# Optimization experiments

Measured on AMD Instinct MI355X. Metric: run time of the kernel, lower is better.

## Reference

```python
import jax, jax.numpy as jnp
import numpy as np

NEG = -1e30  # finite stand-in for -inf so logsumexp grads stay finite


def ctc_loss_mean(y_true, log_probs_tm, input_length, label_length, blank=0):
    """CTC loss (forward algorithm in log space), mean over batch.

    log_probs_tm: [T, B, C] time-major log-probabilities.
    y_true:       [B, L] dense int labels (blank=0 excluded from real labels).
    """
    T, B, C = log_probs_tm.shape
    L = y_true.shape[1]
    S = 2 * L + 1  # extended label length: blank, l1, blank, l2, ...
    ll = jnp.clip(label_length, 1, L)
    il = jnp.clip(input_length, 1, T)

    # Extended label sequence: blanks at even positions, labels at odd.
    ext = jnp.full((B, S), blank, dtype=jnp.int32).at[:, 1::2].set(y_true.astype(jnp.int32))
    ext_m2 = jnp.concatenate([jnp.full((B, 2), -1, jnp.int32), ext[:, :-2]], axis=1)
    # Skip transition (s-2 -> s) allowed only for label positions with no repeat.
    allow_skip = ((jnp.arange(S) % 2 == 1)[None, :]) & (ext != ext_m2)

    lp0 = jnp.take_along_axis(log_probs_tm[0], ext, axis=1)  # [B, S]
    alpha0 = jnp.full((B, S), NEG, log_probs_tm.dtype)
    alpha0 = alpha0.at[:, 0].set(lp0[:, 0]).at[:, 1].set(lp0[:, 1])

    def step(alpha, xs):
        lp_t, t = xs
        lpe = jnp.take_along_axis(lp_t, ext, axis=1)  # [B, S]
        a1 = jnp.concatenate([jnp.full((B, 1), NEG, alpha.dtype), alpha[:, :-1]], axis=1)
        a2 = jnp.concatenate([jnp.full((B, 2), NEG, alpha.dtype), alpha[:, :-2]], axis=1)
        a2 = jnp.where(allow_skip, a2, NEG)
        new = jax.nn.logsumexp(jnp.stack([alpha, a1, a2]), axis=0) + lpe
        # Freeze alpha once past each example's input_length.
        return jnp.where((t < il)[:, None], new, alpha), None

    alpha, _ = jax.lax.scan(step, alpha0, (log_probs_tm[1:], jnp.arange(1, T)))

    # Loss = -log(alpha[2*ll-1] + alpha[2*ll]) at the final (frozen) time step.
    idx = jnp.stack([2 * ll - 1, 2 * ll], axis=1)  # [B, 2]
    end_vals = jnp.take_along_axis(alpha, idx, axis=1)
    loss = -jax.nn.logsumexp(end_vals, axis=1)
    return jnp.mean(loss)


def setup_inputs() -> dict:
    key = jax.random.key(0)
    kx, kl, ki, kj = jax.random.split(key, 4)
    B, T, C, L = 64, 1024, 128, 256
    # y_pred are probabilities (module applies log), so softmax random logits.
    y_pred = jax.nn.softmax(jax.random.normal(kx, (B, T, C), jnp.float32), axis=-1)
    y_true = jax.random.randint(kl, (B, L), 1, C, jnp.int32)  # blank=0 excluded
    input_length = jax.random.randint(ki, (B,), T // 2, T + 1, jnp.int32)
    label_length = jax.random.randint(kj, (B,), L // 2, L + 1, jnp.int32)
    return {"y_true": y_true, "y_pred": y_pred,
            "input_length": input_length, "label_length": label_length}


def reference(y_true, y_pred, input_length, label_length):
    # Mirror CTCLayer.call: log + transpose to time-major, reshape lengths.
    log_tm = jnp.log(jnp.transpose(y_pred, (1, 0, 2)))  # [T, B, C]
    loss = ctc_loss_mean(y_true, log_tm,
                         input_length.reshape(-1), label_length.reshape(-1),
                         blank=0)
    return log_tm, loss
```

## Files before the change

kernel.cpp:

```cpp
#include <hip/hip_runtime.h>
#include <math.h>

constexpr int B = 64;
constexpr int T = 1024;
constexpr int C = 128;
constexpr int L = 256;
constexpr int S = 2 * L + 1;
constexpr int TRB = 2048;

template <int N> struct IC { static constexpr int value = N; };

__device__ __forceinline__ float shr1(float x) {
#if __has_builtin(__builtin_amdgcn_mov_dpp)
    return __int_as_float(__builtin_amdgcn_mov_dpp(
        __float_as_int(x), 0x138 , 0xf, 0xf, true));
#else
    return __int_as_float(__builtin_amdgcn_update_dpp(
        0, __float_as_int(x), 0x138, 0xf, 0xf, true));
#endif
}

template <int CTRL>
__device__ __forceinline__ float maxdpp(float x) {
#if __has_builtin(__builtin_amdgcn_mov_dpp)
    float t = __int_as_float(__builtin_amdgcn_mov_dpp(
        __float_as_int(x), CTRL, 0xf, 0xf, true));
#else
    float t = __int_as_float(__builtin_amdgcn_update_dpp(
        0, __float_as_int(x), CTRL, 0xf, 0xf, true));
#endif
    return fmaxf(x, t);
}

__device__ __forceinline__ float wave_max_dpp(float x) {
    x = maxdpp<0x111>(x);
    x = maxdpp<0x112>(x);
    x = maxdpp<0x114>(x);
    x = maxdpp<0x118>(x);
    x = maxdpp<0x142>(x);
    x = maxdpp<0x143>(x);
    return __int_as_float(__builtin_amdgcn_readlane(__float_as_int(x), 63));
}

__global__
__attribute__((amdgpu_waves_per_eu(1, 1)))
__launch_bounds__(64)
void ctc_fused(
    const float* __restrict__ yp,
    const int*   __restrict__ yt,
    const int*   __restrict__ il_,
    const int*   __restrict__ ll_,
    float* __restrict__ out_log,
    float* __restrict__ out_loss)
{
    const int lane = threadIdx.x;
    if (blockIdx.x >= B) {
        int id = blockIdx.x - B;
        int bb = id >> 5;
        int ck = id & 31;
        const float4* src = (const float4*)yp + ((size_t)bb * T + ck * 32) * 32;
        float4* o4 = (float4*)out_log;
        #pragma unroll
        for (int k = 0; k < 16; ++k) {
            int o = k * 64 + lane;
            float4 v = src[o];
            int tt = ck * 32 + (o >> 5);
            int c4 = o & 31;
            float4 r;
            r.x = __logf(v.x); r.y = __logf(v.y);
            r.z = __logf(v.z); r.w = __logf(v.w);
            o4[((size_t)tt * B + bb) * 32 + c4] = r;
        }
        return;
    }

    const int b = blockIdx.x;

    __shared__ float afin[S];

    int il = il_[b]; il = min(max(il, 1), T);
    int ll = ll_[b]; ll = min(max(ll, 1), L);
    const float* yb = yp + (size_t)b * T * C;

    int4 y4  = *(const int4*)(yt + b * L + 4 * lane);
    int  po  = lane ? 4 * lane - 4 : 0;
    int4 py4 = *(const int4*)(yt + b * L + po);
    int  ppw = yt[b * L + (lane >= 2 ? 4 * lane - 5 : 0)];

    int lab[8]   = {py4.x, py4.y, py4.z, py4.w, y4.x, y4.y, y4.z, y4.w};
    int labm1[8] = {ppw,   py4.x, py4.y, py4.z, py4.w, y4.x, y4.y, y4.z};
    float skf[8];
    #pragma unroll
    for (int k = 0; k < 8; ++k)
        skf[k] = ((4 * lane + k >= 5) && (lab[k] != labm1[k])) ? 1.f : 0.f;

    const int c0 = y4.x, c1 = y4.y, c2 = y4.z, c3 = y4.w;

    int z0;
    asm volatile("v_mov_b32 %0, 0" : "=v"(z0));

    float gv[3][4][4], gbv[3][4];

    auto fill = [&](auto Qc, int r0) {
        constexpr int Q = decltype(Qc)::value;
        #pragma unroll
        for (int j = 0; j < 4; ++j) {
            int r = r0 + j; r = r < T ? r : T - 1;
            const float* rb = yb + (size_t)r * C;
            gbv[Q][j]   = rb[z0];
            gv[Q][j][0] = rb[c0];
            gv[Q][j][1] = rb[c1];
            gv[Q][j][2] = rb[c2];
            gv[Q][j][3] = rb[c3];
        }
    };

    float p00 = yb[0];
    float p0l = yb[c0];

    fill(IC<0>{}, 1);
    fill(IC<1>{}, 5);

    float w[17];
    #pragma unroll
    for (int i = 0; i < 17; ++i) w[i] = 0.f;
    if (lane == 0) { w[8] = p00; w[9] = p0l; }

    auto halo = [&]() {
        #pragma unroll
        for (int k = 0; k < 8; ++k) w[k] = shr1(w[8 + k]);
    };
    halo();

    int lsi = 0;
    int t0 = 0;

    auto group = [&](auto Pc) {
        constexpr int P = decltype(Pc)::value;
        constexpr int F = (P + 2) % 3;
        float g1[4], g2[4], g3[4];
        #pragma unroll
        for (int j = 0; j < 4; ++j) {
            g1[j] = shr1(gv[P][j][1]);
            g2[j] = shr1(gv[P][j][2]);
            g3[j] = shr1(gv[P][j][3]);
        }
        #pragma unroll
        for (int j = 0; j < 4; ++j) {
            #pragma unroll
            for (int i = 16; i >= 2 * (j + 1); --i) {
                float acc = w[i] + w[i - 1];
                float g;
                if (i & 1) {
                    const int k = (i - 1) >> 1;
                    acc = fmaf(skf[k], w[i - 2], acc);
                    g = (k >= 4) ? gv[P][j][k - 4]
                                 : (k == 1 ? g1[j] : (k == 2 ? g2[j] : g3[j]));
                } else {
                    g = gbv[P][j];
                }
                w[i] = acc * g;
            }
        }
        fill(IC<F>{}, t0 + 9);
        __builtin_amdgcn_sched_barrier(0x7);
        halo();
        t0 += 4;
    };

    auto maxw = [&]() {
        return fmaxf(fmaxf(fmaxf(w[8], w[9]), fmaxf(w[10], w[11])),
                     fmaxf(fmaxf(w[12], w[13]),
                           fmaxf(fmaxf(w[14], w[15]), w[16])));
    };

    int pinv_bits = 127 << 23;
    int psh = 0;
    auto measure = [&]() {
        float mm = wave_max_dpp(maxw());
        int eb = (__float_as_int(mm) >> 23) & 0xff;
        int sh = 350 - eb;
        sh = sh > 254 ? 254 : (sh < 1 ? 1 : sh);
        pinv_bits = sh << 23;
        psh = sh - 127;
    };
    auto apply = [&]() {
        float inv = __int_as_float(pinv_bits);
        #pragma unroll
        for (int i = 0; i < 17; ++i) w[i] *= inv;
        lsi -= psh;
    };
    auto rescale = [&]() { measure(); apply(); };

    const int full_end = ((il - 1) >> 2) << 2;

    while (t0 + 24 <= full_end) {
        group(IC<0>{});
        apply();
        group(IC<1>{});
        measure();
        group(IC<2>{});
        apply();
        group(IC<0>{});
        measure();
        group(IC<1>{});
        apply();
        group(IC<2>{});
        measure();
    }
    apply();

    if (t0 + 4 <= full_end) { group(IC<0>{}); rescale(); }
    if (t0 + 4 <= full_end) { group(IC<1>{}); rescale(); }
    if (t0 + 4 <= full_end) { group(IC<2>{}); rescale(); }
    if (t0 + 4 <= full_end) { group(IC<0>{}); rescale(); }
    if (t0 + 4 <= full_end) { group(IC<1>{}); }

    const int ph = (full_end >> 2) % 3;
    float tg[3][4], tb[3];
    switch (ph) {
    case 0:
        #pragma unroll
        for (int j = 0; j < 3; ++j) { tb[j]=gbv[0][j]; tg[j][0]=gv[0][j][0]; tg[j][1]=gv[0][j][1]; tg[j][2]=gv[0][j][2]; tg[j][3]=gv[0][j][3]; }
        break;
    case 1:
        #pragma unroll
        for (int j = 0; j < 3; ++j) { tb[j]=gbv[1][j]; tg[j][0]=gv[1][j][0]; tg[j][1]=gv[1][j][1]; tg[j][2]=gv[1][j][2]; tg[j][3]=gv[1][j][3]; }
        break;
    default:
        #pragma unroll
        for (int j = 0; j < 3; ++j) { tb[j]=gbv[2][j]; tg[j][0]=gv[2][j][0]; tg[j][1]=gv[2][j][1]; tg[j][2]=gv[2][j][2]; tg[j][3]=gv[2][j][3]; }
        break;
    }
    #pragma unroll
    for (int j = 0; j < 3; ++j) {
        int r = full_end + 1 + j;
        if (r < il) {
            float hh = shr1(w[15]);
            float gb = tb[j];
            float n8  = (w[8] + hh) * gb;
            float n9  = fmaf(skf[4], hh,    w[9]  + w[8])  * tg[j][0];
            float n10 = (w[10] + w[9])  * gb;
            float n11 = fmaf(skf[5], w[9],  w[11] + w[10]) * tg[j][1];
            float n12 = (w[12] + w[11]) * gb;
            float n13 = fmaf(skf[6], w[11], w[13] + w[12]) * tg[j][2];
            float n14 = (w[14] + w[13]) * gb;
            float n15 = fmaf(skf[7], w[13], w[15] + w[14]) * tg[j][3];
            float n16 = (w[16] + w[15]) * gb;
            w[8] = n8;  w[9] = n9;  w[10] = n10; w[11] = n11; w[12] = n12;
            w[13] = n13; w[14] = n14; w[15] = n15; w[16] = n16;
        }
    }

    #pragma unroll
    for (int k = 0; k < 8; ++k) afin[8 * lane + k] = w[8 + k];
    if (lane == 63) afin[512] = w[16];
    __syncthreads();
    if (lane == 0) {
        float e1 = afin[2 * ll - 1];
        float e2 = afin[2 * ll];
        float sum = fmaxf(e1 + e2, 1e-37f);
        float loss = -(__log2f(sum) + (float)lsi) * 0.6931471805599453f;
        atomicAdd(out_loss, loss * (1.0f / (float)B));
    }
}

extern "C" void kernel_launch(void* const* d_in, const int* in_sizes, int n_in,
                              void* d_out, int out_size, void* d_ws, size_t ws_size,
                              hipStream_t stream) {
    const int*   y_true = (const int*)d_in[0];
    const float* y_pred = (const float*)d_in[1];
    const int*   in_len = (const int*)d_in[2];
    const int*   lb_len = (const int*)d_in[3];

    float* out_log  = (float*)d_out;
    float* out_loss = (float*)d_out + (size_t)T * B * C;

    hipMemsetAsync(out_loss, 0, sizeof(float), stream);
    ctc_fused<<<B + TRB, 64, 0, stream>>>(y_pred, y_true, in_len, lb_len,
                                          out_log, out_loss);
}
```

Before: 177.4 us.

## Replace 4-step halo window recursion with per-step DPP neighbor shuffle

Each group used to recompute a 17-wide overlapping window, doing redundant halo work across 4 time steps, then refreshed 8 halo values and 3×4 gathered probabilities with DPP shifts. The main loop now runs a 9-value per-step update that fetches one neighbor value per step with a DPP shift. This cuts the redundant arithmetic by roughly half. The cost is one cross-lane dependency per step on the serial critical path, where before there was one per four steps. Row loads now use a single clamped base pointer with constant offsets, and the tail selection shifts its indices to match.

```diff
diff --git a/kernel.cpp b/kernel.cpp
--- a/kernel.cpp
+++ b/kernel.cpp
@@ -82,17 +82,13 @@
     int ll = ll_[b]; ll = min(max(ll, 1), L);
     const float* yb = yp + (size_t)b * T * C;
 
-    int4 y4  = *(const int4*)(yt + b * L + 4 * lane);
-    int  po  = lane ? 4 * lane - 4 : 0;
-    int4 py4 = *(const int4*)(yt + b * L + po);
-    int  ppw = yt[b * L + (lane >= 2 ? 4 * lane - 5 : 0)];
-
-    int lab[8]   = {py4.x, py4.y, py4.z, py4.w, y4.x, y4.y, y4.z, y4.w};
-    int labm1[8] = {ppw,   py4.x, py4.y, py4.z, py4.w, y4.x, y4.y, y4.z};
-    float skf[8];
-    #pragma unroll
-    for (int k = 0; k < 8; ++k)
-        skf[k] = ((4 * lane + k >= 5) && (lab[k] != labm1[k])) ? 1.f : 0.f;
+    int4 y4 = *(const int4*)(yt + b * L + 4 * lane);
+    int  pw = yt[b * L + (lane ? 4 * lane - 1 : 0)];
+
+    float skf4 = (lane && (y4.x != pw))   ? 1.f : 0.f;
+    float skf5 = (y4.y != y4.x) ? 1.f : 0.f;
+    float skf6 = (y4.z != y4.y) ? 1.f : 0.f;
+    float skf7 = (y4.w != y4.z) ? 1.f : 0.f;
 
     const int c0 = y4.x, c1 = y4.y, c2 = y4.z, c3 = y4.w;
 
@@ -103,15 +99,15 @@
 
     auto fill = [&](auto Qc, int r0) {
         constexpr int Q = decltype(Qc)::value;
+        int r = r0 < T - 4 ? r0 : T - 4;
+        const float* rb = yb + (size_t)r * C;
         #pragma unroll
         for (int j = 0; j < 4; ++j) {
-            int r = r0 + j; r = r < T ? r : T - 1;
-            const float* rb = yb + (size_t)r * C;
-            gbv[Q][j]   = rb[z0];
-            gv[Q][j][0] = rb[c0];
-            gv[Q][j][1] = rb[c1];
-            gv[Q][j][2] = rb[c2];
-            gv[Q][j][3] = rb[c3];
+            gbv[Q][j]   = rb[j * C + z0];
+            gv[Q][j][0] = rb[j * C + c0];
+            gv[Q][j][1] = rb[j * C + c1];
+            gv[Q][j][2] = rb[j * C + c2];
+            gv[Q][j][3] = rb[j * C + c3];
         }
     };
 
@@ -121,57 +117,45 @@
     fill(IC<0>{}, 1);
     fill(IC<1>{}, 5);
 
-    float w[17];
+    float a[9];
     #pragma unroll
-    for (int i = 0; i < 17; ++i) w[i] = 0.f;
-    if (lane == 0) { w[8] = p00; w[9] = p0l; }
-
-    auto halo = [&]() {
-        #pragma unroll
-        for (int k = 0; k < 8; ++k) w[k] = shr1(w[8 + k]);
-    };
-    halo();
+    for (int i = 0; i < 9; ++i) a[i] = 0.f;
+    if (lane == 0) { a[0] = p00; a[1] = p0l; }
 
     int lsi = 0;
     int t0 = 0;
+
+    auto step = [&](float gb, float g0, float g1, float g2, float g3) {
+        float hh = shr1(a[7]);
+        float n0 = (a[0] + hh)                      * gb;
+        float n1 = fmaf(skf4, hh,   a[1] + a[0])    * g0;
+        float n2 = (a[2] + a[1])                    * gb;
+        float n3 = fmaf(skf5, a[1], a[3] + a[2])    * g1;
+        float n4 = (a[4] + a[3])                    * gb;
+        float n5 = fmaf(skf6, a[3], a[5] + a[4])    * g2;
+        float n6 = (a[6] + a[5])                    * gb;
+        float n7 = fmaf(skf7, a[5], a[7] + a[6])    * g3;
+        float n8 = (a[8] + a[7])                    * gb;
+        a[0] = n0; a[1] = n1; a[2] = n2; a[3] = n3; a[4] = n4;
+        a[5] = n5; a[6] = n6; a[7] = n7; a[8] = n8;
+    };
 
     auto group = [&](auto Pc) {
         constexpr int P = decltype(Pc)::value;
         constexpr int F = (P + 2) % 3;
-        float g1[4], g2[4], g3[4];
-        #pragma unroll
-        for (int j = 0; j < 4; ++j) {
-            g1[j] = shr1(gv[P][j][1]);
-            g2[j] = shr1(gv[P][j][2]);
-            g3[j] = shr1(gv[P][j][3]);
-        }
-        #pragma unroll
-        for (int j = 0; j < 4; ++j) {
-            #pragma unroll
-            for (int i = 16; i >= 2 * (j + 1); --i) {
-                float acc = w[i] + w[i - 1];
-                float g;
-                if (i & 1) {
-                    const int k = (i - 1) >> 1;
-                    acc = fmaf(skf[k], w[i - 2], acc);
-                    g = (k >= 4) ? gv[P][j][k - 4]
-                                 : (k == 1 ? g1[j] : (k == 2 ? g2[j] : g3[j]));
-                } else {
-                    g = gbv[P][j];
-                }
-                w[i] = acc * g;
-            }
-        }
+        #pragma unroll
+        for (int j = 0; j < 4; ++j)
+            step(gbv[P][j], gv[P][j][0], gv[P][j][1], gv[P][j][2], gv[P][j][3]);
         fill(IC<F>{}, t0 + 9);
         __builtin_amdgcn_sched_barrier(0x7);
-        halo();
         t0 += 4;
     };
 
     auto maxw = [&]() {
-        return fmaxf(fmaxf(fmaxf(w[8], w[9]), fmaxf(w[10], w[11])),
-                     fmaxf(fmaxf(w[12], w[13]),
-                           fmaxf(fmaxf(w[14], w[15]), w[16])));
+        float m0 = fmaxf(fmaxf(a[0], a[1]), a[2]);
+        float m1 = fmaxf(fmaxf(a[3], a[4]), a[5]);
+        float m2 = fmaxf(fmaxf(a[6], a[7]), a[8]);
+        return fmaxf(fmaxf(m0, m1), m2);
     };
 
     int pinv_bits = 127 << 23;
@@ -187,7 +171,7 @@
     auto apply = [&]() {
         float inv = __int_as_float(pinv_bits);
         #pragma unroll
-        for (int i = 0; i < 17; ++i) w[i] *= inv;
+        for (int i = 0; i < 9; ++i) a[i] *= inv;
         lsi -= psh;
     };
     auto rescale = [&]() { measure(); apply(); };
@@ -216,45 +200,33 @@
     if (t0 + 4 <= full_end) { group(IC<0>{}); rescale(); }
     if (t0 + 4 <= full_end) { group(IC<1>{}); }
 
-    const int ph = (full_end >> 2) % 3;
+    const int ph  = (full_end >> 2) % 3;
+    const int tsh = (full_end + 1 > T - 4) ? 1 : 0;
     float tg[3][4], tb[3];
     switch (ph) {
     case 0:
         #pragma unroll
-        for (int j = 0; j < 3; ++j) { tb[j]=gbv[0][j]; tg[j][0]=gv[0][j][0]; tg[j][1]=gv[0][j][1]; tg[j][2]=gv[0][j][2]; tg[j][3]=gv[0][j][3]; }
+        for (int j = 0; j < 3; ++j) { int s_ = j + tsh; tb[j]=gbv[0][s_]; tg[j][0]=gv[0][s_][0]; tg[j][1]=gv[0][s_][1]; tg[j][2]=gv[0][s_][2]; tg[j][3]=gv[0][s_][3]; }
         break;
     case 1:
         #pragma unroll
-        for (int j = 0; j < 3; ++j) { tb[j]=gbv[1][j]; tg[j][0]=gv[1][j][0]; tg[j][1]=gv[1][j][1]; tg[j][2]=gv[1][j][2]; tg[j][3]=gv[1][j][3]; }
+        for (int j = 0; j < 3; ++j) { int s_ = j + tsh; tb[j]=gbv[1][s_]; tg[j][0]=gv[1][s_][0]; tg[j][1]=gv[1][s_][1]; tg[j][2]=gv[1][s_][2]; tg[j][3]=gv[1][s_][3]; }
         break;
     default:
         #pragma unroll
-        for (int j = 0; j < 3; ++j) { tb[j]=gbv[2][j]; tg[j][0]=gv[2][j][0]; tg[j][1]=gv[2][j][1]; tg[j][2]=gv[2][j][2]; tg[j][3]=gv[2][j][3]; }
+        for (int j = 0; j < 3; ++j) { int s_ = j + tsh; tb[j]=gbv[2][s_]; tg[j][0]=gv[2][s_][0]; tg[j][1]=gv[2][s_][1]; tg[j][2]=gv[2][s_][2]; tg[j][3]=gv[2][s_][3]; }
         break;
     }
     #pragma unroll
     for (int j = 0; j < 3; ++j) {
         int r = full_end + 1 + j;
-        if (r < il) {
-            float hh = shr1(w[15]);
-            float gb = tb[j];
-            float n8  = (w[8] + hh) * gb;
-            float n9  = fmaf(skf[4], hh,    w[9]  + w[8])  * tg[j][0];
-            float n10 = (w[10] + w[9])  * gb;
-            float n11 = fmaf(skf[5], w[9],  w[11] + w[10]) * tg[j][1];
-            float n12 = (w[12] + w[11]) * gb;
-            float n13 = fmaf(skf[6], w[11], w[13] + w[12]) * tg[j][2];
-            float n14 = (w[14] + w[13]) * gb;
-            float n15 = fmaf(skf[7], w[13], w[15] + w[14]) * tg[j][3];
-            float n16 = (w[16] + w[15]) * gb;
-            w[8] = n8;  w[9] = n9;  w[10] = n10; w[11] = n11; w[12] = n12;
-            w[13] = n13; w[14] = n14; w[15] = n15; w[16] = n16;
-        }
+        if (r < il)
+            step(tb[j], tg[j][0], tg[j][1], tg[j][2], tg[j][3]);
     }
 
     #pragma unroll
-    for (int k = 0; k < 8; ++k) afin[8 * lane + k] = w[8 + k];
-    if (lane == 63) afin[512] = w[16];
+    for (int k = 0; k < 8; ++k) afin[8 * lane + k] = a[k];
+    if (lane == 63) afin[512] = a[8];
     __syncthreads();
     if (lane == 0) {
         float e1 = afin[2 * ll - 1];
```

Measured after the change: 171.2 us. -3.5%, faster.
